# Kernel tuning notes

Measured on AMD Instinct MI355X. Metric: run time of the kernel, lower is better.

The kernel has to match this reference:

```python
import jax, jax.numpy as jnp
import numpy as np

FP8_MAX = 448.0  # float8_e4m3fn max
EPS = 1e-6


def _rms_norm(x, w):
    # x: [T, H], w: [H]
    var = jnp.mean(x * x, axis=-1, keepdims=True)
    return x * jax.lax.rsqrt(var + EPS) * w


def _fused_add_rms_norm(x, resid, w):
    r = x + resid
    return _rms_norm(r, w), r


def _fp8_linear(y, W):
    # dynamic per-token activation quant + per-tensor weight quant, fp8 e4m3
    s = jnp.maximum(jnp.max(jnp.abs(y), axis=-1, keepdims=True) / FP8_MAX, 1e-12)  # [T,1]
    qx = jnp.clip(y / s, -FP8_MAX, FP8_MAX).astype(jnp.float8_e4m3fn).astype(jnp.float32)
    ws = jnp.maximum(jnp.max(jnp.abs(W)) / FP8_MAX, 1e-12)  # scalar
    qw = jnp.clip(W / ws, -FP8_MAX, FP8_MAX).astype(jnp.float8_e4m3fn).astype(jnp.float32)
    # out = dequant(qx) @ dequant(qw).T = (qx @ qw.T) * s * ws ; W is [out, in]
    return (qx @ qw.T) * (s * ws)


def setup_inputs() -> dict:
    key = jax.random.key(0)
    ks = jax.random.split(key, 8)
    H, T = 4096, 4096
    x = jax.random.normal(ks[0], (T, H), dtype=jnp.float32)
    nw0 = 1.0 + 0.02 * jax.random.normal(ks[1], (H,), dtype=jnp.float32)
    nw1 = 1.0 + 0.02 * jax.random.normal(ks[2], (H,), dtype=jnp.float32)
    nw2 = 1.0 + 0.02 * jax.random.normal(ks[3], (H,), dtype=jnp.float32)
    nw3 = 1.0 + 0.02 * jax.random.normal(ks[4], (H,), dtype=jnp.float32)
    W0 = 0.02 * jax.random.normal(ks[5], (H, H), dtype=jnp.float32)
    W1 = 0.02 * jax.random.normal(ks[6], (H, H), dtype=jnp.float32)
    W2 = 0.02 * jax.random.normal(ks[7], (H, H), dtype=jnp.float32)
    return {"x": x, "nw0": nw0, "nw1": nw1, "nw2": nw2, "nw3": nw3,
            "W0": W0, "W1": W1, "W2": W2}


def reference(x, nw0, nw1, nw2, nw3, W0, W1, W2):
    x = jax.nn.relu(x)
    resid = x
    y = _rms_norm(x, nw0)
    x2 = _fp8_linear(y, W0)
    y2, resid = _fused_add_rms_norm(x2, resid, nw1)
    x3 = _fp8_linear(y2, W1)
    y3, resid = _fused_add_rms_norm(x3, resid, nw2)
    x4 = _fp8_linear(y3, W2)
    y4, resid = _fused_add_rms_norm(x4, resid, nw3)
    return y4
```

## Files before the change

kernel.cpp:

```cpp
#include <hip/hip_runtime.h>
#include <cstdint>
#include <cstddef>

#define AS1 __attribute__((address_space(1)))
#define AS3 __attribute__((address_space(3)))

typedef __attribute__((ext_vector_type(4))) float f32x4;
typedef __attribute__((ext_vector_type(16))) float f32x16;
typedef __attribute__((ext_vector_type(4))) int i32x4;
typedef __attribute__((ext_vector_type(8))) int i32x8;

constexpr int HD = 4096;
constexpr float FP8MAX = 448.0f;

__device__ inline uint32_t pack4_fp8(float a, float b, float c, float d) {
    int v = 0;
    v = __builtin_amdgcn_cvt_pk_fp8_f32(a, b, v, false);
    v = __builtin_amdgcn_cvt_pk_fp8_f32(c, d, v, true);
    return (uint32_t)v;
}

__device__ inline float clipmul(float y, float rcs) {
    float t = y * rcs;
    t = fminf(t, FP8MAX);
    t = fmaxf(t, -FP8MAX);
    return t;
}

__device__ inline uint32_t quant4(float4 v, float rcs) {
    return pack4_fp8(clipmul(v.x, rcs), clipmul(v.y, rcs),
                     clipmul(v.z, rcs), clipmul(v.w, rcs));
}

__device__ inline float max4(float4 v) {
    return fmaxf(fmaxf(fabsf(v.x), fabsf(v.y)), fmaxf(fabsf(v.z), fabsf(v.w)));
}

__global__ __launch_bounds__(256) void w_absmax(const float* __restrict__ W0,
                                                const float* __restrict__ W1,
                                                const float* __restrict__ W2,
                                                uint32_t* __restrict__ wmax) {
    __shared__ float red[4];
    const float* W = (blockIdx.z == 0) ? W0 : (blockIdx.z == 1 ? W1 : W2);
    const float4* W4 = (const float4*)W;
    const int n4 = HD * HD / 4;
    float m = 0.f;
    for (int i = blockIdx.x * blockDim.x + threadIdx.x; i < n4; i += gridDim.x * blockDim.x) {
        m = fmaxf(m, max4(W4[i]));
    }
#pragma unroll
    for (int i = 32; i > 0; i >>= 1) m = fmaxf(m, __shfl_xor(m, i, 64));
    if ((threadIdx.x & 63) == 0) red[threadIdx.x >> 6] = m;
    __syncthreads();
    if (threadIdx.x == 0) {
        m = fmaxf(fmaxf(red[0], red[1]), fmaxf(red[2], red[3]));
        atomicMax((unsigned int*)(wmax + blockIdx.z), __float_as_uint(m));
    }
}

__global__ __launch_bounds__(256) void w_absmax1(const float* __restrict__ W,
                                                 uint32_t* __restrict__ slot) {
    __shared__ float red[4];
    const float4* W4 = (const float4*)W;
    const int stride = 2048 * 256;
    int i = blockIdx.x * 256 + threadIdx.x;
    float a0 = 0.f, a1 = 0.f, a2 = 0.f, a3 = 0.f;
#pragma unroll
    for (int it = 0; it < 2; it++) {
        float4 v0 = W4[i];
        float4 v1 = W4[i + stride];
        float4 v2 = W4[i + 2 * stride];
        float4 v3 = W4[i + 3 * stride];
        a0 = fmaxf(a0, max4(v0));
        a1 = fmaxf(a1, max4(v1));
        a2 = fmaxf(a2, max4(v2));
        a3 = fmaxf(a3, max4(v3));
        i += 4 * stride;
    }
    float m = fmaxf(fmaxf(a0, a1), fmaxf(a2, a3));
#pragma unroll
    for (int s = 32; s > 0; s >>= 1) m = fmaxf(m, __shfl_xor(m, s, 64));
    if ((threadIdx.x & 63) == 0) red[threadIdx.x >> 6] = m;
    __syncthreads();
    if (threadIdx.x == 0) {
        m = fmaxf(fmaxf(red[0], red[1]), fmaxf(red[2], red[3]));
        atomicMax((unsigned int*)slot, __float_as_uint(m));
    }
}

__global__ __launch_bounds__(256) void w_quant(const float* __restrict__ W,
                                               const uint32_t* __restrict__ wmaxbits,
                                               uint32_t* __restrict__ qw) {
    const float rsw = 1.0f / fmaxf(__uint_as_float(*wmaxbits) / FP8MAX, 1e-12f);
    const int i = blockIdx.x * blockDim.x + threadIdx.x;
    qw[i] = quant4(((const float4*)W)[i], rsw);
}

__global__ __launch_bounds__(256) void fused_rms(const float* __restrict__ xin,
                                                 float* __restrict__ resid_out,
                                                 const float* __restrict__ nw,
                                                 uint32_t* __restrict__ qx,
                                                 float* __restrict__ srow,
                                                 float* __restrict__ yout,
                                                 const int mode,
                                                 const float* __restrict__ Wq,
                                                 const uint32_t* __restrict__ wqmaxbits,
                                                 uint32_t* __restrict__ qwout,
                                                 const float* __restrict__ Wa1,
                                                 const float* __restrict__ Wa2,
                                                 uint32_t* __restrict__ wmaxbase) {
    const int tid = threadIdx.x;
    __shared__ float reds[4];
    __shared__ float redm[4];

    if (blockIdx.x >= 8192) {
        const int b = blockIdx.x - 8192;
        const float* W = (b < 512) ? Wa1 : Wa2;
        uint32_t* slot = wmaxbase + ((b < 512) ? 1 : 2);
        const int bb = b & 511;
        const float4* W4 = (const float4*)W;
        const int stride = 512 * 256;
        int i = bb * 256 + tid;
        float a0 = 0.f, a1 = 0.f, a2 = 0.f, a3 = 0.f;
#pragma unroll
        for (int it = 0; it < 8; it++) {
            float4 v0 = W4[i];
            float4 v1 = W4[i + stride];
            float4 v2 = W4[i + 2 * stride];
            float4 v3 = W4[i + 3 * stride];
            a0 = fmaxf(a0, max4(v0));
            a1 = fmaxf(a1, max4(v1));
            a2 = fmaxf(a2, max4(v2));
            a3 = fmaxf(a3, max4(v3));
            i += 4 * stride;
        }
        float m = fmaxf(fmaxf(a0, a1), fmaxf(a2, a3));
#pragma unroll
        for (int s = 32; s > 0; s >>= 1) m = fmaxf(m, __shfl_xor(m, s, 64));
        if ((tid & 63) == 0) reds[tid >> 6] = m;
        __syncthreads();
        if (tid == 0) {
            m = fmaxf(fmaxf(reds[0], reds[1]), fmaxf(reds[2], reds[3]));
            atomicMax((unsigned int*)slot, __float_as_uint(m));
        }
        return;
    }

    if (blockIdx.x >= 4096) {
        const float rsw = 1.0f / fmaxf(__uint_as_float(*wqmaxbits) / FP8MAX, 1e-12f);
        const float4* W4 = (const float4*)Wq;
        int i = (blockIdx.x - 4096) * 256 + tid;
#pragma unroll
        for (int it = 0; it < 4; it++, i += 4096 * 256)
            qwout[i] = quant4(W4[i], rsw);
        return;
    }

    const int row = blockIdx.x;
    const size_t base = (size_t)row * HD;
    const float4* xr = (const float4*)(xin + base);
    const float4* nw4 = (const float4*)nw;

    float4 v[4], w[4];
    float ss = 0.f, pm = 0.f;
    if (mode == 0) {
#pragma unroll
        for (int j = 0; j < 4; j++) {
            float4 t = xr[tid + j * 256];
            w[j] = nw4[tid + j * 256];
            t.x = fmaxf(t.x, 0.f); t.y = fmaxf(t.y, 0.f);
            t.z = fmaxf(t.z, 0.f); t.w = fmaxf(t.w, 0.f);
            v[j] = t;
            ss += t.x * t.x + t.y * t.y + t.z * t.z + t.w * t.w;
            pm = fmaxf(pm, fmaxf(fmaxf(fabsf(t.x * w[j].x), fabsf(t.y * w[j].y)),
                                 fmaxf(fabsf(t.z * w[j].z), fabsf(t.w * w[j].w))));
        }
    } else {
#pragma unroll
        for (int j = 0; j < 4; j++) {
            float4 t = xr[tid + j * 256];
            w[j] = nw4[tid + j * 256];
            v[j] = t;
            ss += t.x * t.x + t.y * t.y + t.z * t.z + t.w * t.w;
            pm = fmaxf(pm, fmaxf(fmaxf(fabsf(t.x * w[j].x), fabsf(t.y * w[j].y)),
                                 fmaxf(fabsf(t.z * w[j].z), fabsf(t.w * w[j].w))));
        }
    }
    if (resid_out) {
        float4* ro = (float4*)(resid_out + base);
#pragma unroll
        for (int j = 0; j < 4; j++) ro[tid + j * 256] = v[j];
    }

#pragma unroll
    for (int i = 32; i > 0; i >>= 1) {
        ss += __shfl_xor(ss, i, 64);
        pm = fmaxf(pm, __shfl_xor(pm, i, 64));
    }
    if ((tid & 63) == 0) { reds[tid >> 6] = ss; redm[tid >> 6] = pm; }
    __syncthreads();
    ss = (reds[0] + reds[1]) + (reds[2] + reds[3]);
    pm = fmaxf(fmaxf(redm[0], redm[1]), fmaxf(redm[2], redm[3]));

    const float rs = 1.0f / sqrtf(ss / (float)HD + 1e-6f);

    if (mode == 2) {
        float4* yo = (float4*)(yout + base);
#pragma unroll
        for (int j = 0; j < 4; j++) {
            float4 t;
            t.x = (v[j].x * rs) * w[j].x; t.y = (v[j].y * rs) * w[j].y;
            t.z = (v[j].z * rs) * w[j].z; t.w = (v[j].w * rs) * w[j].w;
            yo[tid + j * 256] = t;
        }
        return;
    }

    const float amax = pm * rs;
    const float s = fmaxf(amax / FP8MAX, 1e-12f);
    const float rcs = 1.0f / s;
    if (tid == 0) srow[row] = s;
    uint32_t* qr = qx + base / 4;
#pragma unroll
    for (int j = 0; j < 4; j++) {
        float4 t;
        t.x = (v[j].x * rs) * w[j].x; t.y = (v[j].y * rs) * w[j].y;
        t.z = (v[j].z * rs) * w[j].z; t.w = (v[j].w * rs) * w[j].w;
        qr[tid + j * 256] = quant4(t, rcs);
    }
}

typedef union { i32x8 v8; i32x4 v4[2]; } frag8;

__global__ __launch_bounds__(512, 2) void gemm_fp8mx(const uint8_t* __restrict__ qx,
                                                     const uint8_t* __restrict__ qw,
                                                     const float* __restrict__ srow,
                                                     const uint32_t* __restrict__ wmaxbits,
                                                     float* resid) {
    __shared__ i32x4 AsL[2][2][1024];
    __shared__ i32x4 BsL[2][2][1024];

    const int tid = threadIdx.x;
    const int wave = tid >> 6, lane = tid & 63;
    const int lr = lane & 31, lh = lane >> 5;
    const int m0 = blockIdx.y * 256, n0 = blockIdx.x * 256;
    const int wm = (wave >> 2) * 128, wn = (wave & 3) * 64;

    const int str = tid >> 2;
    const int skg = (tid & 3) ^ ((str >> 1) & 3);
    const size_t srcA = (size_t)(m0 + str) * HD + (size_t)(skg * 16);
    const size_t srcB = (size_t)(n0 + str) * HD + (size_t)(skg * 16);

    f32x16 acc[4][2];
#pragma unroll
    for (int i = 0; i < 4; i++)
#pragma unroll
        for (int j = 0; j < 2; j++)
#pragma unroll
            for (int e = 0; e < 16; e++) acc[i][j][e] = 0.f;

    frag8 af0, af1, af2, af3, bf0, bf1;

#define STAGE_U(gp, soff, larr, koff) do {                                              \
    __builtin_amdgcn_global_load_lds((const AS1 void*)((gp) + (soff) + (size_t)(koff)), \
                                     (AS3 void*)((larr) + tid), 16, 0, 0);              \
    __builtin_amdgcn_global_load_lds((const AS1 void*)((gp) + (soff) + (size_t)(koff) + 128u * HD), \
                                     (AS3 void*)((larr) + 512 + tid), 16, 0, 0);        \
} while (0)

#define READ_F(dst, rbase, larr) do {                 \
    const int r_ = (rbase);                           \
    const i32x4* p_ = (larr) + r_ * 4;                \
    const int sw_ = (r_ >> 1) & 3;                    \
    dst.v4[0] = p_[(lh * 2) ^ sw_];                   \
    dst.v4[1] = p_[(lh * 2 + 1) ^ sw_];               \
} while (0)

#define MFMA1(a_, b_, i_, j_)                                                            \
    acc[i_][j_] = __builtin_amdgcn_mfma_scale_f32_32x32x64_f8f6f4(                       \
        (a_).v8, (b_).v8, acc[i_][j_], 0, 0, 0, 0x7F7F7F7Fu, 0, 0x7F7F7F7Fu)

#define MFMA4(a0_, a1_, r0_, r1_) do {               \
    __builtin_amdgcn_s_setprio(1);                   \
    MFMA1(a0_, bf0, r0_, 0);                         \
    MFMA1(a0_, bf1, r0_, 1);                         \
    MFMA1(a1_, bf0, r1_, 0);                         \
    MFMA1(a1_, bf1, r1_, 1);                         \
    __builtin_amdgcn_s_setprio(0);                   \
} while (0)

#define KHALF(bR, bS, kh, knext) do {                               \
                             \
    READ_F(af0, wm + lr,      &AsL[bR][kh][0]);                     \
    READ_F(af1, wm + 32 + lr, &AsL[bR][kh][0]);                     \
    READ_F(bf0, wn + lr,      &BsL[bR][kh][0]);                     \
    READ_F(bf1, wn + 32 + lr, &BsL[bR][kh][0]);                     \
    READ_F(af2, wm + 64 + lr, &AsL[bR][kh][0]);                     \
    READ_F(af3, wm + 96 + lr, &AsL[bR][kh][0]);                     \
    STAGE_U(qx, srcA, &AsL[bS][kh][0], (knext));                    \
    __builtin_amdgcn_s_barrier();                                   \
    MFMA4(af0, af1, 0, 1);                                          \
    __builtin_amdgcn_s_barrier();                                   \
    STAGE_U(qw, srcB, &BsL[bS][kh][0], (knext));                    \
    __builtin_amdgcn_s_barrier();                                   \
    MFMA4(af2, af3, 2, 3);                                          \
    asm volatile("s_waitcnt vmcnt(4)" ::: "memory");                \
    __builtin_amdgcn_s_barrier();                                   \
} while (0)

#define KTILE(bR, bS, knext) do {                                   \
    KHALF(bR, bS, 0, (knext));                                      \
    KHALF(bR, bS, 1, (knext) + 64);                                 \
} while (0)

    STAGE_U(qx, srcA, &AsL[0][0][0], 0);
    STAGE_U(qw, srcB, &BsL[0][0][0], 0);
    STAGE_U(qx, srcA, &AsL[0][1][0], 64);
    STAGE_U(qw, srcB, &BsL[0][1][0], 64);
    asm volatile("s_waitcnt vmcnt(4)" ::: "memory");
    __builtin_amdgcn_s_barrier();

#pragma unroll 1
    for (int kt = 0; kt < 32; kt += 2) {
        KTILE(0, 1, (kt + 1) * 128);
        KTILE(1, 0, ((kt + 2) & 31) * 128);
    }

    const float wsc = fmaxf(__uint_as_float(*wmaxbits) / FP8MAX, 1e-12f);
#pragma unroll
    for (int i = 0; i < 4; i++) {
#pragma unroll
        for (int reg = 0; reg < 16; reg++) {
            const int row = (reg & 3) + 8 * (reg >> 2) + 4 * lh;
            const int m = m0 + wm + i * 32 + row;
            const float sv = srow[m] * wsc;
            float* orow = resid + (size_t)m * HD + n0 + wn + lr;
#pragma unroll
            for (int j = 0; j < 2; j++)
                orow[j * 32] = acc[i][j][reg] * sv + orow[j * 32];
        }
    }
#undef KTILE
#undef KHALF
#undef MFMA4
#undef MFMA1
#undef READ_F
#undef STAGE_U
}

extern "C" void kernel_launch(void* const* d_in, const int* in_sizes, int n_in,
                              void* d_out, int out_size, void* d_ws, size_t ws_size,
                              hipStream_t stream) {
    const float* x   = (const float*)d_in[0];
    const float* nw0 = (const float*)d_in[1];
    const float* nw1 = (const float*)d_in[2];
    const float* nw2 = (const float*)d_in[3];
    const float* nw3 = (const float*)d_in[4];
    const float* W0  = (const float*)d_in[5];
    const float* W1  = (const float*)d_in[6];
    const float* W2  = (const float*)d_in[7];
    float* out = (float*)d_out;

    char* ws = (char*)d_ws;
    const size_t MB = 1024 * 1024;

    const bool overlap = ws_size >= 118 * MB;

    if (overlap) {
        float*    resid = (float*)(ws);
        uint32_t* qx    = (uint32_t*)(ws + 64 * MB);
        uint32_t* qwA   = (uint32_t*)(ws + 80 * MB);
        uint32_t* qwB   = (uint32_t*)(ws + 96 * MB);
        float*    srow  = (float*)(ws + 112 * MB);
        uint32_t* wmax  = (uint32_t*)(ws + 112 * MB + 16384);

        hipMemsetAsync(wmax, 0, 12, stream);
        hipLaunchKernelGGL(w_absmax1, dim3(2048), dim3(256), 0, stream, W0, wmax + 0);

        hipLaunchKernelGGL(fused_rms, dim3(9216), dim3(256), 0, stream,
                           x, resid, nw0, qx, srow, (float*)nullptr, 0,
                           W0, wmax + 0, qwA, W1, W2, wmax);
        hipLaunchKernelGGL(gemm_fp8mx, dim3(16, 16), dim3(512), 0, stream,
                           (const uint8_t*)qx, (const uint8_t*)qwA, srow, wmax + 0, resid);
        hipLaunchKernelGGL(fused_rms, dim3(8192), dim3(256), 0, stream,
                           resid, (float*)nullptr, nw1, qx, srow, (float*)nullptr, 1,
                           W1, wmax + 1, qwB,
                           (const float*)nullptr, (const float*)nullptr, (uint32_t*)nullptr);
        hipLaunchKernelGGL(gemm_fp8mx, dim3(16, 16), dim3(512), 0, stream,
                           (const uint8_t*)qx, (const uint8_t*)qwB, srow, wmax + 1, resid);
        hipLaunchKernelGGL(fused_rms, dim3(8192), dim3(256), 0, stream,
                           resid, (float*)nullptr, nw2, qx, srow, (float*)nullptr, 1,
                           W2, wmax + 2, qwA,
                           (const float*)nullptr, (const float*)nullptr, (uint32_t*)nullptr);
        hipLaunchKernelGGL(gemm_fp8mx, dim3(16, 16), dim3(512), 0, stream,
                           (const uint8_t*)qx, (const uint8_t*)qwA, srow, wmax + 2, resid);
        hipLaunchKernelGGL(fused_rms, dim3(4096), dim3(256), 0, stream,
                           resid, (float*)nullptr, nw3,
                           (uint32_t*)nullptr, (float*)nullptr, out, 2,
                           (const float*)nullptr, (const uint32_t*)nullptr, (uint32_t*)nullptr,
                           (const float*)nullptr, (const float*)nullptr, (uint32_t*)nullptr);
    } else {
        float*    resid = (float*)(ws);
        uint32_t* qx    = (uint32_t*)(ws + 64 * MB);
        uint32_t* qw    = (uint32_t*)(ws + 80 * MB);
        float*    srow  = (float*)(ws + 96 * MB);
        uint32_t* wmax  = (uint32_t*)(ws + 96 * MB + 16384);

        hipMemsetAsync(wmax, 0, 12, stream);
        hipLaunchKernelGGL(w_absmax, dim3(1024, 1, 3), dim3(256), 0, stream, W0, W1, W2, wmax);
        hipLaunchKernelGGL(fused_rms, dim3(4096), dim3(256), 0, stream,
                           x, resid, nw0, qx, srow, (float*)nullptr, 0,
                           (const float*)nullptr, (const uint32_t*)nullptr, (uint32_t*)nullptr,
                           (const float*)nullptr, (const float*)nullptr, (uint32_t*)nullptr);
        const float* Ws[3]  = {W0, W1, W2};
        const float* nws[3] = {nw1, nw2, nw3};
        for (int l = 0; l < 3; l++) {
            hipLaunchKernelGGL(w_quant, dim3(HD * HD / 4 / 256), dim3(256), 0, stream,
                               Ws[l], wmax + l, qw);
            hipLaunchKernelGGL(gemm_fp8mx, dim3(16, 16), dim3(512), 0, stream,
                               (const uint8_t*)qx, (const uint8_t*)qw, srow, wmax + l, resid);
            if (l < 2) {
                hipLaunchKernelGGL(fused_rms, dim3(4096), dim3(256), 0, stream,
                                   resid, (float*)nullptr, nws[l], qx, srow,
                                   (float*)nullptr, 1,
                                   (const float*)nullptr, (const uint32_t*)nullptr, (uint32_t*)nullptr,
                                   (const float*)nullptr, (const float*)nullptr, (uint32_t*)nullptr);
            } else {
                hipLaunchKernelGGL(fused_rms, dim3(4096), dim3(256), 0, stream,
                                   resid, (float*)nullptr, nws[l],
                                   (uint32_t*)nullptr, (float*)nullptr, out, 2,
                                   (const float*)nullptr, (const uint32_t*)nullptr, (uint32_t*)nullptr,
                                   (const float*)nullptr, (const float*)nullptr, (uint32_t*)nullptr);
            }
        }
    }
}
```

Before: 629.6 us.

## Remap GEMM tiles per XCD, prefetch residual rows into LDS, merge absmax kernels

The weight absmax for all three layers moves into one kernel launched over three weights, replacing the per-layer absmax blocks that were folded into fused_rms. The GEMM block index is remapped so blocks on the same XCD share nearby output tiles, which should improve L2 reuse. The final k-tile is peeled, and its free LDS slots prefetch part of the residual tile so the epilogue reads those rows from LDS instead of global memory. The order of fragment reads and A staging in KHALF is also adjusted, which adds complexity and risk around waitcnt and barriers.

```diff
diff --git a/kernel.cpp b/kernel.cpp
--- a/kernel.cpp
+++ b/kernel.cpp
@@ -36,31 +36,12 @@
     return fmaxf(fmaxf(fabsf(v.x), fabsf(v.y)), fmaxf(fabsf(v.z), fabsf(v.w)));
 }
 
-__global__ __launch_bounds__(256) void w_absmax(const float* __restrict__ W0,
-                                                const float* __restrict__ W1,
-                                                const float* __restrict__ W2,
-                                                uint32_t* __restrict__ wmax) {
+__global__ __launch_bounds__(256) void w_absmax3(const float* __restrict__ W0,
+                                                 const float* __restrict__ W1,
+                                                 const float* __restrict__ W2,
+                                                 uint32_t* __restrict__ wmax) {
     __shared__ float red[4];
     const float* W = (blockIdx.z == 0) ? W0 : (blockIdx.z == 1 ? W1 : W2);
-    const float4* W4 = (const float4*)W;
-    const int n4 = HD * HD / 4;
-    float m = 0.f;
-    for (int i = blockIdx.x * blockDim.x + threadIdx.x; i < n4; i += gridDim.x * blockDim.x) {
-        m = fmaxf(m, max4(W4[i]));
-    }
-#pragma unroll
-    for (int i = 32; i > 0; i >>= 1) m = fmaxf(m, __shfl_xor(m, i, 64));
-    if ((threadIdx.x & 63) == 0) red[threadIdx.x >> 6] = m;
-    __syncthreads();
-    if (threadIdx.x == 0) {
-        m = fmaxf(fmaxf(red[0], red[1]), fmaxf(red[2], red[3]));
-        atomicMax((unsigned int*)(wmax + blockIdx.z), __float_as_uint(m));
-    }
-}
-
-__global__ __launch_bounds__(256) void w_absmax1(const float* __restrict__ W,
-                                                 uint32_t* __restrict__ slot) {
-    __shared__ float red[4];
     const float4* W4 = (const float4*)W;
     const int stride = 2048 * 256;
     int i = blockIdx.x * 256 + threadIdx.x;
@@ -84,7 +65,7 @@
     __syncthreads();
     if (threadIdx.x == 0) {
         m = fmaxf(fmaxf(red[0], red[1]), fmaxf(red[2], red[3]));
-        atomicMax((unsigned int*)slot, __float_as_uint(m));
+        atomicMax((unsigned int*)(wmax + blockIdx.z), __float_as_uint(m));
     }
 }
 
@@ -105,46 +86,10 @@
                                                  const int mode,
                                                  const float* __restrict__ Wq,
                                                  const uint32_t* __restrict__ wqmaxbits,
-                                                 uint32_t* __restrict__ qwout,
-                                                 const float* __restrict__ Wa1,
-                                                 const float* __restrict__ Wa2,
-                                                 uint32_t* __restrict__ wmaxbase) {
+                                                 uint32_t* __restrict__ qwout) {
     const int tid = threadIdx.x;
     __shared__ float reds[4];
     __shared__ float redm[4];
-
-    if (blockIdx.x >= 8192) {
-        const int b = blockIdx.x - 8192;
-        const float* W = (b < 512) ? Wa1 : Wa2;
-        uint32_t* slot = wmaxbase + ((b < 512) ? 1 : 2);
-        const int bb = b & 511;
-        const float4* W4 = (const float4*)W;
-        const int stride = 512 * 256;
-        int i = bb * 256 + tid;
-        float a0 = 0.f, a1 = 0.f, a2 = 0.f, a3 = 0.f;
-#pragma unroll
-        for (int it = 0; it < 8; it++) {
-            float4 v0 = W4[i];
-            float4 v1 = W4[i + stride];
-            float4 v2 = W4[i + 2 * stride];
-            float4 v3 = W4[i + 3 * stride];
-            a0 = fmaxf(a0, max4(v0));
-            a1 = fmaxf(a1, max4(v1));
-            a2 = fmaxf(a2, max4(v2));
-            a3 = fmaxf(a3, max4(v3));
-            i += 4 * stride;
-        }
-        float m = fmaxf(fmaxf(a0, a1), fmaxf(a2, a3));
-#pragma unroll
-        for (int s = 32; s > 0; s >>= 1) m = fmaxf(m, __shfl_xor(m, s, 64));
-        if ((tid & 63) == 0) reds[tid >> 6] = m;
-        __syncthreads();
-        if (tid == 0) {
-            m = fmaxf(fmaxf(reds[0], reds[1]), fmaxf(reds[2], reds[3]));
-            atomicMax((unsigned int*)slot, __float_as_uint(m));
-        }
-        return;
-    }
 
     if (blockIdx.x >= 4096) {
         const float rsw = 1.0f / fmaxf(__uint_as_float(*wqmaxbits) / FP8MAX, 1e-12f);
@@ -243,7 +188,12 @@
     const int tid = threadIdx.x;
     const int wave = tid >> 6, lane = tid & 63;
     const int lr = lane & 31, lh = lane >> 5;
-    const int m0 = blockIdx.y * 256, n0 = blockIdx.x * 256;
+
+    const int bid = blockIdx.y * 16 + blockIdx.x;
+    const int xcd = bid & 7, jj = bid >> 3;
+    const int bx = (xcd & 3) * 4 + (jj & 3);
+    const int by = (xcd >> 2) * 8 + (jj >> 2);
+    const int m0 = by * 256, n0 = bx * 256;
     const int wm = (wave >> 2) * 128, wn = (wave & 3) * 64;
 
     const int str = tid >> 2;
@@ -266,6 +216,16 @@
                                      (AS3 void*)((larr) + tid), 16, 0, 0);              \
     __builtin_amdgcn_global_load_lds((const AS1 void*)((gp) + (soff) + (size_t)(koff) + 128u * HD), \
                                      (AS3 void*)((larr) + 512 + tid), 16, 0, 0);        \
+} while (0)
+
+#define RSTAGE(u) do {                                                                  \
+    const int byte_ = (u) * 8192 + tid * 16;                                            \
+    const int rr_ = byte_ >> 10;                                                        \
+    const int cb_ = byte_ & 1023;                                                       \
+    const uint8_t* s_ = (const uint8_t*)resid + ((size_t)(m0 + rr_) * HD + n0) * 4 + cb_; \
+    uint8_t* d_ = ((u) < 4 ? (uint8_t*)&AsL[0][0][0] + (u) * 8192                       \
+                           : (uint8_t*)&BsL[0][0][0] + ((u) - 4) * 8192) + tid * 16;    \
+    __builtin_amdgcn_global_load_lds((const AS1 void*)s_, (AS3 void*)d_, 16, 0, 0);     \
 } while (0)
 
 #define READ_F(dst, rbase, larr) do {                 \
@@ -290,17 +250,16 @@
 } while (0)
 
 #define KHALF(bR, bS, kh, knext) do {                               \
-                             \
     READ_F(af0, wm + lr,      &AsL[bR][kh][0]);                     \
     READ_F(af1, wm + 32 + lr, &AsL[bR][kh][0]);                     \
     READ_F(bf0, wn + lr,      &BsL[bR][kh][0]);                     \
     READ_F(bf1, wn + 32 + lr, &BsL[bR][kh][0]);                     \
+    STAGE_U(qx, srcA, &AsL[bS][kh][0], (knext));                    \
+    __builtin_amdgcn_s_barrier();                                   \
+    MFMA4(af0, af1, 0, 1);                                          \
+    __builtin_amdgcn_s_barrier();                                   \
     READ_F(af2, wm + 64 + lr, &AsL[bR][kh][0]);                     \
     READ_F(af3, wm + 96 + lr, &AsL[bR][kh][0]);                     \
-    STAGE_U(qx, srcA, &AsL[bS][kh][0], (knext));                    \
-    __builtin_amdgcn_s_barrier();                                   \
-    MFMA4(af0, af1, 0, 1);                                          \
-    __builtin_amdgcn_s_barrier();                                   \
     STAGE_U(qw, srcB, &BsL[bS][kh][0], (knext));                    \
     __builtin_amdgcn_s_barrier();                                   \
     MFMA4(af2, af3, 2, 3);                                          \
@@ -311,6 +270,24 @@
 #define KTILE(bR, bS, knext) do {                                   \
     KHALF(bR, bS, 0, (knext));                                      \
     KHALF(bR, bS, 1, (knext) + 64);                                 \
+} while (0)
+
+#define KHALF_LAST(kh, u0, LASTWAIT) do {                           \
+    READ_F(af0, wm + lr,      &AsL[1][kh][0]);                      \
+    READ_F(af1, wm + 32 + lr, &AsL[1][kh][0]);                      \
+    READ_F(bf0, wn + lr,      &BsL[1][kh][0]);                      \
+    READ_F(bf1, wn + 32 + lr, &BsL[1][kh][0]);                      \
+    RSTAGE((u0)); RSTAGE((u0) + 1);                                 \
+    __builtin_amdgcn_s_barrier();                                   \
+    MFMA4(af0, af1, 0, 1);                                          \
+    __builtin_amdgcn_s_barrier();                                   \
+    READ_F(af2, wm + 64 + lr, &AsL[1][kh][0]);                      \
+    READ_F(af3, wm + 96 + lr, &AsL[1][kh][0]);                      \
+    RSTAGE((u0) + 2); RSTAGE((u0) + 3);                             \
+    __builtin_amdgcn_s_barrier();                                   \
+    MFMA4(af2, af3, 2, 3);                                          \
+    asm volatile(LASTWAIT ::: "memory");                            \
+    __builtin_amdgcn_s_barrier();                                   \
 } while (0)
 
     STAGE_U(qx, srcA, &AsL[0][0][0], 0);
@@ -321,10 +298,13 @@
     __builtin_amdgcn_s_barrier();
 
 #pragma unroll 1
-    for (int kt = 0; kt < 32; kt += 2) {
+    for (int kt = 0; kt < 30; kt += 2) {
         KTILE(0, 1, (kt + 1) * 128);
-        KTILE(1, 0, ((kt + 2) & 31) * 128);
-    }
+        KTILE(1, 0, (kt + 2) * 128);
+    }
+    KTILE(0, 1, 31 * 128);
+    KHALF_LAST(0, 0, "s_waitcnt vmcnt(4)");
+    KHALF_LAST(1, 4, "s_waitcnt vmcnt(0)");
 
     const float wsc = fmaxf(__uint_as_float(*wmaxbits) / FP8MAX, 1e-12f);
 #pragma unroll
@@ -332,19 +312,32 @@
 #pragma unroll
         for (int reg = 0; reg < 16; reg++) {
             const int row = (reg & 3) + 8 * (reg >> 2) + 4 * lh;
-            const int m = m0 + wm + i * 32 + row;
+            const int lrow = wm + i * 32 + row;
+            const int m = m0 + lrow;
             const float sv = srow[m] * wsc;
             float* orow = resid + (size_t)m * HD + n0 + wn + lr;
 #pragma unroll
-            for (int j = 0; j < 2; j++)
-                orow[j * 32] = acc[i][j][reg] * sv + orow[j * 32];
+            for (int j = 0; j < 2; j++) {
+                float rv;
+                if (lrow < 64) {
+                    const int fb = lrow * 1024 + (wn + lr + j * 32) * 4;
+                    rv = (fb < 32768)
+                         ? *(const float*)((const uint8_t*)&AsL[0][0][0] + fb)
+                         : *(const float*)((const uint8_t*)&BsL[0][0][0] + (fb - 32768));
+                } else {
+                    rv = orow[j * 32];
+                }
+                orow[j * 32] = acc[i][j][reg] * sv + rv;
+            }
         }
     }
 #undef KTILE
 #undef KHALF
+#undef KHALF_LAST
 #undef MFMA4
 #undef MFMA1
 #undef READ_F
+#undef RSTAGE
 #undef STAGE_U
 }
 
@@ -375,30 +368,27 @@
         uint32_t* wmax  = (uint32_t*)(ws + 112 * MB + 16384);
 
         hipMemsetAsync(wmax, 0, 12, stream);
-        hipLaunchKernelGGL(w_absmax1, dim3(2048), dim3(256), 0, stream, W0, wmax + 0);
-
-        hipLaunchKernelGGL(fused_rms, dim3(9216), dim3(256), 0, stream,
+        hipLaunchKernelGGL(w_absmax3, dim3(2048, 1, 3), dim3(256), 0, stream, W0, W1, W2, wmax);
+
+        hipLaunchKernelGGL(fused_rms, dim3(8192), dim3(256), 0, stream,
                            x, resid, nw0, qx, srow, (float*)nullptr, 0,
-                           W0, wmax + 0, qwA, W1, W2, wmax);
+                           W0, wmax + 0, qwA);
         hipLaunchKernelGGL(gemm_fp8mx, dim3(16, 16), dim3(512), 0, stream,
                            (const uint8_t*)qx, (const uint8_t*)qwA, srow, wmax + 0, resid);
         hipLaunchKernelGGL(fused_rms, dim3(8192), dim3(256), 0, stream,
                            resid, (float*)nullptr, nw1, qx, srow, (float*)nullptr, 1,
-                           W1, wmax + 1, qwB,
-                           (const float*)nullptr, (const float*)nullptr, (uint32_t*)nullptr);
+                           W1, wmax + 1, qwB);
         hipLaunchKernelGGL(gemm_fp8mx, dim3(16, 16), dim3(512), 0, stream,
                            (const uint8_t*)qx, (const uint8_t*)qwB, srow, wmax + 1, resid);
         hipLaunchKernelGGL(fused_rms, dim3(8192), dim3(256), 0, stream,
                            resid, (float*)nullptr, nw2, qx, srow, (float*)nullptr, 1,
-                           W2, wmax + 2, qwA,
-                           (const float*)nullptr, (const float*)nullptr, (uint32_t*)nullptr);
+                           W2, wmax + 2, qwA);
         hipLaunchKernelGGL(gemm_fp8mx, dim3(16, 16), dim3(512), 0, stream,
                            (const uint8_t*)qx, (const uint8_t*)qwA, srow, wmax + 2, resid);
         hipLaunchKernelGGL(fused_rms, dim3(4096), dim3(256), 0, stream,
                            resid, (float*)nullptr, nw3,
                            (uint32_t*)nullptr, (float*)nullptr, out, 2,
-                           (const float*)nullptr, (const uint32_t*)nullptr, (uint32_t*)nullptr,
-                           (const float*)nullptr, (const float*)nullptr, (uint32_t*)nullptr);
+                           (const float*)nullptr, (const uint32_t*)nullptr, (uint32_t*)nullptr);
     } else {
         float*    resid = (float*)(ws);
         uint32_t* qx    = (uint32_t*)(ws + 64 * MB);
@@ -407,11 +397,10 @@
         uint32_t* wmax  = (uint32_t*)(ws + 96 * MB + 16384);
 
         hipMemsetAsync(wmax, 0, 12, stream);
-        hipLaunchKernelGGL(w_absmax, dim3(1024, 1, 3), dim3(256), 0, stream, W0, W1, W2, wmax);
+        hipLaunchKernelGGL(w_absmax3, dim3(2048, 1, 3), dim3(256), 0, stream, W0, W1, W2, wmax);
         hipLaunchKernelGGL(fused_rms, dim3(4096), dim3(256), 0, stream,
                            x, resid, nw0, qx, srow, (float*)nullptr, 0,
-                           (const float*)nullptr, (const uint32_t*)nullptr, (uint32_t*)nullptr,
-                           (const float*)nullptr, (const float*)nullptr, (uint32_t*)nullptr);
+                           (const float*)nullptr, (const uint32_t*)nullptr, (uint32_t*)nullptr);
         const float* Ws[3]  = {W0, W1, W2};
         const float* nws[3] = {nw1, nw2, nw3};
         for (int l = 0; l < 3; l++) {
@@ -423,14 +412,12 @@
                 hipLaunchKernelGGL(fused_rms, dim3(4096), dim3(256), 0, stream,
                                    resid, (float*)nullptr, nws[l], qx, srow,
                                    (float*)nullptr, 1,
-                                   (const float*)nullptr, (const uint32_t*)nullptr, (uint32_t*)nullptr,
-                                   (const float*)nullptr, (const float*)nullptr, (uint32_t*)nullptr);
+                                   (const float*)nullptr, (const uint32_t*)nullptr, (uint32_t*)nullptr);
             } else {
                 hipLaunchKernelGGL(fused_rms, dim3(4096), dim3(256), 0, stream,
                                    resid, (float*)nullptr, nws[l],
                                    (uint32_t*)nullptr, (float*)nullptr, out, 2,
-                                   (const float*)nullptr, (const uint32_t*)nullptr, (uint32_t*)nullptr,
-                                   (const float*)nullptr, (const float*)nullptr, (uint32_t*)nullptr);
+                                   (const float*)nullptr, (const uint32_t*)nullptr, (uint32_t*)nullptr);
             }
         }
     }
```

Measured after the change: 641.9 us. About the same (+1.9%).
